# Performance work log

Measured on AMD Instinct MI355X. Metric: run time of the kernel, lower is better.

The kernel has to match this reference:

```python
import jax, jax.numpy as jnp
import numpy as np

N = 131072          # total rows across all types
IN_C = 512          # in_channels
OUT_C = 512         # out_channels
NUM_TYPES = 8       # len(types)


def setup_inputs() -> dict:
    key = jax.random.key(0)
    k1, k2, k3, k4 = jax.random.split(key, 4)
    x = jax.random.normal(k1, (N, IN_C), dtype=jnp.float32)
    type_vec = jnp.sort(jax.random.randint(k2, (N,), 0, NUM_TYPES)).astype(jnp.int64)
    # HeteroLinear params: weight [num_types, in, out], bias [num_types, out]
    scale = 1.0 / np.sqrt(IN_C)
    weight = jax.random.normal(k3, (NUM_TYPES, IN_C, OUT_C), dtype=jnp.float32) * scale
    bias = jax.random.normal(k4, (NUM_TYPES, OUT_C), dtype=jnp.float32) * scale
    return {"x": x, "type_vec": type_vec, "weight": weight, "bias": bias}


def _grouped_linear(x, type_vec, weight, bias):
    """out[n] = x[n] @ weight[type_vec[n]] + bias[type_vec[n]].

    Computed as T masked dense GEMMs (T is small) to avoid gathering a
    [N, in, out] per-row weight tensor.
    """
    n, out_c = x.shape[0], weight.shape[2]

    def per_type(acc, t):
        mask = (type_vec == t).astype(x.dtype)[:, None]  # [N, 1]
        y = (x * mask) @ weight[t] + mask * bias[t]      # [N, out]
        return acc + y, None

    out, _ = jax.lax.scan(per_type,
                          jnp.zeros((n, out_c), dtype=x.dtype),
                          jnp.arange(weight.shape[0]))
    return out


def reference(x, type_vec, weight, bias):
    # Equivalent to ToHeteroLinear.fused_forward (and dict_forward after the
    # cat/repeat_interleave, since type_vec is sorted / is_sorted=True).
    return _grouped_linear(x, type_vec, weight, bias)
```

## Files before the change

### kernel.cpp

```cpp
#include <hip/hip_runtime.h>

#define NROWS 131072
#define KDIM 512
#define NDIM 512

using short8  = __attribute__((ext_vector_type(8))) short;
using float4v = __attribute__((ext_vector_type(4))) float;
using uint4v  = __attribute__((ext_vector_type(4))) unsigned int;

__device__ __forceinline__ unsigned pack_trunc(float a, float b) {
    unsigned ua = __builtin_bit_cast(unsigned, a);
    unsigned ub = __builtin_bit_cast(unsigned, b);
    return __builtin_amdgcn_perm(ub, ua, 0x07060302u);
}
__device__ __forceinline__ unsigned pack_round(float a, float b) {
    unsigned ua = __builtin_bit_cast(unsigned, a) + 0x8000u;
    unsigned ub = __builtin_bit_cast(unsigned, b) + 0x8000u;
    return __builtin_amdgcn_perm(ub, ua, 0x07060302u);
}

__global__ __launch_bounds__(256) void wconv_kernel(const float* __restrict__ w,
                                                    unsigned short* __restrict__ wt) {
    int b  = blockIdx.x;
    int ty = b >> 6;
    int ot = (b >> 3) & 7;
    int it = b & 7;
    __shared__ float tile[64][65];
    const float* wp = w + ((size_t)ty << 18);
    int tid = threadIdx.x;
    int cf = tid & 15, ir0 = tid >> 4;
    #pragma unroll
    for (int j = 0; j < 4; ++j) {
        int ir = ir0 + 16 * j;
        float4v v = *(const float4v*)(wp + (size_t)(it * 64 + ir) * NDIM + ot * 64 + cf * 4);
        tile[ir][cf * 4 + 0] = v.x;
        tile[ir][cf * 4 + 1] = v.y;
        tile[ir][cf * 4 + 2] = v.z;
        tile[ir][cf * 4 + 3] = v.w;
    }
    __syncthreads();
    int oc = tid >> 2, iq = tid & 3;
    unsigned* op = (unsigned*)(wt + ((size_t)ty << 18) + (size_t)(ot * 64 + oc) * KDIM + it * 64 + iq * 16);
    #pragma unroll
    for (int j = 0; j < 8; ++j)
        op[j] = pack_round(tile[iq * 16 + 2 * j][oc], tile[iq * 16 + 2 * j + 1][oc]);
}

__global__ __launch_bounds__(256, 2)
void hetero_gemm_kernel(const float* __restrict__ x,
                        const int* __restrict__ tv,
                        const unsigned short* __restrict__ wt,
                        const float* __restrict__ bias,
                        float* __restrict__ out) {
    __shared__ uint4v ldsA[4 * 128];
    __shared__ uint4v ldsB[4 * 128];

    const int b = blockIdx.x;
    const int rowTile = ((b >> 5) << 3) | (b & 7);
    const int colTile = (b >> 3) & 3;
    const int row0 = rowTile << 7;
    const int col0 = colTile << 7;

    const int tid  = threadIdx.x;
    const int lane = tid & 63;
    const int wave = tid >> 6;
    const int wm   = (wave & 1) << 6;
    const int wn   = (wave >> 1) << 6;
    const int l15  = lane & 15;
    const int quad = lane >> 4;

    const int ra = tid >> 1;
    const int khalf = tid & 1;
    const int rtypeA = tv[row0 + ra];

    const int nb = tid & 127;
    const int g2 = tid >> 7;

    const int t0 = tv[row0];
    const int t1 = tv[row0 + 127];

    float4v acc[4][4];
    float4v zero = {0.f, 0.f, 0.f, 0.f};
    #pragma unroll
    for (int i = 0; i < 4; ++i)
        #pragma unroll
        for (int j = 0; j < 4; ++j)
            acc[i][j] = zero;

    for (int tt = t0; tt <= t1; ++tt) {
        const unsigned maskA = (rtypeA == tt) ? 0xFFFFFFFFu : 0u;
        const float* ap = x + (size_t)(row0 + ra) * KDIM + khalf * 16;
        const unsigned short* wb = wt + ((size_t)tt << 18) + (size_t)(col0 + nb) * KDIM;

        float4v av[4];
        uint4v  bv[2];
        #pragma unroll
        for (int i = 0; i < 4; ++i) av[i] = *(const float4v*)(ap + i * 4);
        bv[0] = *(const uint4v*)(wb + g2 * 8);
        bv[1] = *(const uint4v*)(wb + (g2 + 2) * 8);

        for (int kc = 0; kc < KDIM; kc += 32) {
            __syncthreads();
            uint4v pa0, pa1;
            pa0.x = pack_trunc(av[0].x, av[0].y) & maskA;
            pa0.y = pack_trunc(av[0].z, av[0].w) & maskA;
            pa0.z = pack_trunc(av[1].x, av[1].y) & maskA;
            pa0.w = pack_trunc(av[1].z, av[1].w) & maskA;
            pa1.x = pack_trunc(av[2].x, av[2].y) & maskA;
            pa1.y = pack_trunc(av[2].z, av[2].w) & maskA;
            pa1.z = pack_trunc(av[3].x, av[3].y) & maskA;
            pa1.w = pack_trunc(av[3].z, av[3].w) & maskA;
            ldsA[(khalf * 2 + 0) * 128 + ra] = pa0;
            ldsA[(khalf * 2 + 1) * 128 + ra] = pa1;
            ldsB[(g2    ) * 128 + nb] = bv[0];
            ldsB[(g2 + 2) * 128 + nb] = bv[1];
            __syncthreads();

            if (kc + 32 < KDIM) {
                const float* ap2 = ap + kc + 32;
                #pragma unroll
                for (int i = 0; i < 4; ++i) av[i] = *(const float4v*)(ap2 + i * 4);
                const unsigned short* wb2 = wb + kc + 32;
                bv[0] = *(const uint4v*)(wb2 + g2 * 8);
                bv[1] = *(const uint4v*)(wb2 + (g2 + 2) * 8);
            }

            short8 af[4], bf[4];
            #pragma unroll
            for (int mi = 0; mi < 4; ++mi)
                af[mi] = *(const short8*)&ldsA[quad * 128 + wm + mi * 16 + l15];
            #pragma unroll
            for (int ni = 0; ni < 4; ++ni)
                bf[ni] = *(const short8*)&ldsB[quad * 128 + wn + ni * 16 + l15];
            #pragma unroll
            for (int mi = 0; mi < 4; ++mi)
                #pragma unroll
                for (int ni = 0; ni < 4; ++ni)
                    acc[mi][ni] = __builtin_amdgcn_mfma_f32_16x16x32_bf16(
                        af[mi], bf[ni], acc[mi][ni], 0, 0, 0);
        }
    }

    #pragma unroll
    for (int mi = 0; mi < 4; ++mi) {
        #pragma unroll
        for (int r = 0; r < 4; ++r) {
            const int grow = row0 + wm + mi * 16 + quad * 4 + r;
            const int rt = tv[grow];
            const float* brow = bias + (size_t)rt * NDIM;
            float* orow = out + (size_t)grow * NDIM;
            #pragma unroll
            for (int ni = 0; ni < 4; ++ni) {
                const int gcol = col0 + wn + ni * 16 + l15;
                orow[gcol] = acc[mi][ni][r] + brow[gcol];
            }
        }
    }
}

extern "C" void kernel_launch(void* const* d_in, const int* in_sizes, int n_in,
                              void* d_out, int out_size, void* d_ws, size_t ws_size,
                              hipStream_t stream) {
    const float* x    = (const float*)d_in[0];
    const int*   tv   = (const int*)d_in[1];
    const float* w    = (const float*)d_in[2];
    const float* bias = (const float*)d_in[3];
    float* out = (float*)d_out;
    unsigned short* wtr = (unsigned short*)d_ws;

    wconv_kernel<<<512, 256, 0, stream>>>(w, wtr);
    hetero_gemm_kernel<<<4096, 256, 0, stream>>>(x, tv, wtr, bias, out);
}
```

Before: 545.8 us.

## Pre-convert x to bf16 and stream tiles via async global-to-LDS double buffering

Adds a separate pass that converts x to bf16 in workspace. A new GEMM kernel then loads A and B tiles directly into double-buffered, XOR-swizzled LDS with global_load_lds, and applies the per-row type mask only for tiles that span several types. This is meant to cut the fp32 read traffic of x inside the GEMM, remove register-staged LDS stores, and overlap loads with MFMA. In exchange it adds an extra full pass over x (a 256 MB read and 128 MB write) and needs enough workspace. If the workspace is too small it falls back to the old fused kernel.

```diff
diff --git a/kernel.cpp b/kernel.cpp
--- a/kernel.cpp
+++ b/kernel.cpp
@@ -3,6 +3,7 @@
 #define NROWS 131072
 #define KDIM 512
 #define NDIM 512
+#define NTYPES 8
 
 using short8  = __attribute__((ext_vector_type(8))) short;
 using float4v = __attribute__((ext_vector_type(4))) float;
@@ -17,6 +18,13 @@
     unsigned ua = __builtin_bit_cast(unsigned, a) + 0x8000u;
     unsigned ub = __builtin_bit_cast(unsigned, b) + 0x8000u;
     return __builtin_amdgcn_perm(ub, ua, 0x07060302u);
+}
+
+__device__ __forceinline__ void load_lds16(const unsigned short* g, void* l) {
+    __builtin_amdgcn_global_load_lds(
+        (const __attribute__((address_space(1))) unsigned int*)g,
+        (__attribute__((address_space(3))) unsigned int*)l,
+        16, 0, 0);
 }
 
 __global__ __launch_bounds__(256) void wconv_kernel(const float* __restrict__ w,
@@ -46,14 +54,26 @@
         op[j] = pack_round(tile[iq * 16 + 2 * j][oc], tile[iq * 16 + 2 * j + 1][oc]);
 }
 
-__global__ __launch_bounds__(256, 2)
-void hetero_gemm_kernel(const float* __restrict__ x,
-                        const int* __restrict__ tv,
-                        const unsigned short* __restrict__ wt,
-                        const float* __restrict__ bias,
-                        float* __restrict__ out) {
-    __shared__ uint4v ldsA[4 * 128];
-    __shared__ uint4v ldsB[4 * 128];
+__global__ __launch_bounds__(256) void xconv_kernel(const float* __restrict__ x,
+                                                    uint4v* __restrict__ xb) {
+    size_t t = (size_t)blockIdx.x * 256 + threadIdx.x;
+    const float4v* xp = (const float4v*)x + t * 2;
+    float4v a = xp[0], b = xp[1];
+    uint4v p;
+    p.x = pack_round(a.x, a.y);
+    p.y = pack_round(a.z, a.w);
+    p.z = pack_round(b.x, b.y);
+    p.w = pack_round(b.z, b.w);
+    xb[t] = p;
+}
+
+__global__ __launch_bounds__(256)
+void hetero_gemm_bf16(const unsigned short* __restrict__ xb,
+                      const int* __restrict__ tv,
+                      const unsigned short* __restrict__ wt,
+                      const float* __restrict__ bias,
+                      float* __restrict__ out) {
+    __shared__ uint4v lds[2][2][512];
 
     const int b = blockIdx.x;
     const int rowTile = ((b >> 5) << 3) | (b & 7);
@@ -68,11 +88,123 @@
     const int wn   = (wave >> 1) << 6;
     const int l15  = lane & 15;
     const int quad = lane >> 4;
+    const int swz  = quad ^ (l15 & 3);
+
+    const int n0 = tid, n1 = 256 + tid;
+    const int ar0 = n0 >> 2, ak0 = (n0 & 3) ^ (ar0 & 3);
+    const int ar1 = n1 >> 2, ak1 = (n1 & 3) ^ (ar1 & 3);
+    const unsigned short* a0 = xb + (size_t)(row0 + ar0) * KDIM + ak0 * 8;
+    const unsigned short* a1 = xb + (size_t)(row0 + ar1) * KDIM + ak1 * 8;
+
+    const int t0 = tv[row0];
+    const int t1 = tv[row0 + 127];
+    const bool multi = (t0 != t1);
+
+    int rt[4];
+    #pragma unroll
+    for (int mi = 0; mi < 4; ++mi) rt[mi] = tv[row0 + wm + mi * 16 + l15];
+
+    float4v acc[4][4];
+    float4v zero = {0.f, 0.f, 0.f, 0.f};
+    #pragma unroll
+    for (int i = 0; i < 4; ++i)
+        #pragma unroll
+        for (int j = 0; j < 4; ++j)
+            acc[i][j] = zero;
+
+    for (int tt = t0; tt <= t1; ++tt) {
+        const unsigned short* wb = wt + ((size_t)tt << 18);
+        const unsigned short* b0 = wb + (size_t)(col0 + ar0) * KDIM + ak0 * 8;
+        const unsigned short* b1 = wb + (size_t)(col0 + ar1) * KDIM + ak1 * 8;
+
+        unsigned am[4];
+        if (multi) {
+            #pragma unroll
+            for (int mi = 0; mi < 4; ++mi) am[mi] = (rt[mi] == tt) ? 0xFFFFFFFFu : 0u;
+        }
+
+        load_lds16(a0, &lds[0][0][n0]);
+        load_lds16(a1, &lds[0][0][n1]);
+        load_lds16(b0, &lds[0][1][n0]);
+        load_lds16(b1, &lds[0][1][n1]);
+
+        for (int c = 0; c < 16; ++c) {
+            __syncthreads();
+            const int cur = c & 1;
+            if (c < 15) {
+                const int kc = (c + 1) * 32;
+                const int nxt = cur ^ 1;
+                load_lds16(a0 + kc, &lds[nxt][0][n0]);
+                load_lds16(a1 + kc, &lds[nxt][0][n1]);
+                load_lds16(b0 + kc, &lds[nxt][1][n0]);
+                load_lds16(b1 + kc, &lds[nxt][1][n1]);
+            }
+
+            short8 af[4], bf[4];
+            #pragma unroll
+            for (int mi = 0; mi < 4; ++mi) {
+                const int row = wm + mi * 16 + l15;
+                uint4v v = lds[cur][0][(row << 2) | swz];
+                if (multi) { v.x &= am[mi]; v.y &= am[mi]; v.z &= am[mi]; v.w &= am[mi]; }
+                af[mi] = __builtin_bit_cast(short8, v);
+            }
+            #pragma unroll
+            for (int ni = 0; ni < 4; ++ni) {
+                const int col = wn + ni * 16 + l15;
+                bf[ni] = __builtin_bit_cast(short8, lds[cur][1][(col << 2) | swz]);
+            }
+            #pragma unroll
+            for (int mi = 0; mi < 4; ++mi)
+                #pragma unroll
+                for (int ni = 0; ni < 4; ++ni)
+                    acc[mi][ni] = __builtin_amdgcn_mfma_f32_16x16x32_bf16(
+                        af[mi], bf[ni], acc[mi][ni], 0, 0, 0);
+        }
+    }
+
+    #pragma unroll
+    for (int mi = 0; mi < 4; ++mi) {
+        #pragma unroll
+        for (int r = 0; r < 4; ++r) {
+            const int grow = row0 + wm + mi * 16 + quad * 4 + r;
+            const int rtt = tv[grow];
+            const float* brow = bias + (size_t)rtt * NDIM;
+            float* orow = out + (size_t)grow * NDIM;
+            #pragma unroll
+            for (int ni = 0; ni < 4; ++ni) {
+                const int gcol = col0 + wn + ni * 16 + l15;
+                orow[gcol] = acc[mi][ni][r] + brow[gcol];
+            }
+        }
+    }
+}
+
+__global__ __launch_bounds__(256, 2)
+void hetero_gemm_fused(const float* __restrict__ x,
+                       const int* __restrict__ tv,
+                       const unsigned short* __restrict__ wt,
+                       const float* __restrict__ bias,
+                       float* __restrict__ out) {
+    __shared__ uint4v ldsA[4 * 128];
+    __shared__ uint4v ldsB[4 * 128];
+
+    const int b = blockIdx.x;
+    const int rowTile = ((b >> 5) << 3) | (b & 7);
+    const int colTile = (b >> 3) & 3;
+    const int row0 = rowTile << 7;
+    const int col0 = colTile << 7;
+
+    const int tid  = threadIdx.x;
+    const int lane = tid & 63;
+    const int wave = tid >> 6;
+    const int wm   = (wave & 1) << 6;
+    const int wn   = (wave >> 1) << 6;
+    const int l15  = lane & 15;
+    const int quad = lane >> 4;
 
     const int ra = tid >> 1;
     const int khalf = tid & 1;
     const int rtypeA = tv[row0 + ra];
-
     const int nb = tid & 127;
     const int g2 = tid >> 7;
 
@@ -146,8 +278,8 @@
         #pragma unroll
         for (int r = 0; r < 4; ++r) {
             const int grow = row0 + wm + mi * 16 + quad * 4 + r;
-            const int rt = tv[grow];
-            const float* brow = bias + (size_t)rt * NDIM;
+            const int rtt = tv[grow];
+            const float* brow = bias + (size_t)rtt * NDIM;
             float* orow = out + (size_t)grow * NDIM;
             #pragma unroll
             for (int ni = 0; ni < 4; ++ni) {
@@ -166,8 +298,19 @@
     const float* w    = (const float*)d_in[2];
     const float* bias = (const float*)d_in[3];
     float* out = (float*)d_out;
-    unsigned short* wtr = (unsigned short*)d_ws;
-
-    wconv_kernel<<<512, 256, 0, stream>>>(w, wtr);
-    hetero_gemm_kernel<<<4096, 256, 0, stream>>>(x, tv, wtr, bias, out);
-}
+
+    const size_t xb_bytes = (size_t)NROWS * KDIM * 2;
+    const size_t wt_bytes = (size_t)NTYPES * KDIM * NDIM * 2;
+
+    if (ws_size >= xb_bytes + wt_bytes) {
+        unsigned short* xbb = (unsigned short*)d_ws;
+        unsigned short* wtr = (unsigned short*)((char*)d_ws + xb_bytes);
+        wconv_kernel<<<512, 256, 0, stream>>>(w, wtr);
+        xconv_kernel<<<NROWS * KDIM / 8 / 256, 256, 0, stream>>>(x, (uint4v*)xbb);
+        hetero_gemm_bf16<<<4096, 256, 0, stream>>>(xbb, tv, wtr, bias, out);
+    } else {
+        unsigned short* wtr = (unsigned short*)d_ws;
+        wconv_kernel<<<512, 256, 0, stream>>>(w, wtr);
+        hetero_gemm_fused<<<4096, 256, 0, stream>>>(x, tv, wtr, bias, out);
+    }
+}
```

Measured after the change: 571.4 us. 4.7% more time.
